# Kernel optimization log

Hardware: AMD Instinct MI355X
Metric: run time of the kernel (lower is better)

The kernel has to match this reference:

```python
import jax, jax.numpy as jnp
import numpy as np

TEMPERATURE = 0.1
NEG_INF = -1e30


def setup_inputs() -> dict:
    key = jax.random.key(0)
    ks = jax.random.split(key, 8)
    T, B, D = 2048, 16, 256
    inp = {
        'q1': jax.random.normal(ks[0], (T, B, D), dtype=jnp.float32),
        'k2': jax.random.normal(ks[1], (T, B, D), dtype=jnp.float32),
        'q2': jax.random.normal(ks[2], (T, B, D), dtype=jnp.float32),
        'k1': jax.random.normal(ks[3], (T, B, D), dtype=jnp.float32),
        'mask_q1': jnp.ones((B, T), dtype=bool),
        'mask_q2': jnp.ones((B, T), dtype=bool),
        'len_q1': jax.random.randint(ks[4], (B,), 0, T, dtype=jnp.int32),
        'len_k2': jax.random.randint(ks[5], (B,), 0, T, dtype=jnp.int32),
        'len_q2': jax.random.randint(ks[6], (B,), 0, T, dtype=jnp.int32),
        'len_k1': jax.random.randint(ks[7], (B,), 0, T, dtype=jnp.int32),
    }
    return inp


def _compute_loss(pred, target, len_pred, len_target):
    # pred, target: (T, B, D) -> (B, T, D)
    pred = jnp.transpose(pred, (1, 0, 2))
    target = jnp.transpose(target, (1, 0, 2))
    B, T, _ = pred.shape
    min_l = jnp.minimum(len_pred, len_target)  # (B,)

    # Batched truncated matmul realized as full matmul + column masking.
    logits = jnp.einsum('btd,bsd->bts', pred, target) / TEMPERATURE  # (B, T, T)
    idx = jnp.arange(T)
    col_valid = idx[None, None, :] < min_l[:, None, None]
    logits = jnp.where(col_valid, logits, NEG_INF)

    # Cross-entropy with labels = arange(min_l): loss_i = lse_i - logits[i, i]
    lse = jax.nn.logsumexp(logits, axis=-1)                 # (B, T)
    diag = jnp.diagonal(logits, axis1=1, axis2=2)           # (B, T)
    row_loss = lse - diag

    row_valid = idx[None, :] < min_l[:, None]               # (B, T)
    denom = jnp.maximum(min_l, 1).astype(pred.dtype)
    per_sample = jnp.sum(jnp.where(row_valid, row_loss, 0.0), axis=1) / denom

    valid = min_l > 0
    n_valid = jnp.sum(valid.astype(pred.dtype))
    total = jnp.sum(jnp.where(valid, per_sample, 0.0))
    return jnp.where(n_valid > 0, total / jnp.maximum(n_valid, 1.0), 0.0)


def reference(q1, k2, q2, k1, mask_q1, mask_q2, len_q1, len_k2, len_q2, len_k1):
    # masks are unused in the original math (kept for interface fidelity)
    loss_a = _compute_loss(q1, k2, len_q1, len_k2)
    loss_b = _compute_loss(q2, k1, len_q2, len_k1)
    return (loss_a + loss_b) / 2
```

## Files before the change

### kernel.cpp

```cpp
#include <hip/hip_runtime.h>
#include <hip/hip_bf16.h>
#include <cmath>

#define T_DIM 2048
#define B_DIM 16
#define D_DIM 256
#define BD (B_DIM * D_DIM)
#define ROWU 256
#define SLAB (T_DIM * ROWU)
#define BM 128
#define BN 64
#define NS 8
#define CHUNK (T_DIM / NS)
#define NEG_INF_F (-1e30f)
#define SCALE_LOG2 14.4269504088896f
#define LN2F 0.6931471805599453f

typedef __attribute__((ext_vector_type(8))) short bf16x8;
typedef __attribute__((ext_vector_type(8))) unsigned short ushort8;
typedef __attribute__((ext_vector_type(4))) float f32x4;

static __device__ __forceinline__ ushort f2bf(float f) {
    union { float f; unsigned int u; } x; x.f = f;
    unsigned int r = (x.u + 0x7FFFu + ((x.u >> 16) & 1u)) >> 16;
    return (ushort)r;
}

static __device__ __forceinline__ void gload_lds16(const ushort* g, ushort* l) {
    __builtin_amdgcn_global_load_lds(
        (const __attribute__((address_space(1))) unsigned int*)g,
        (__attribute__((address_space(3))) unsigned int*)l,
        16, 0, 0);
}

__global__ __launch_bounds__(256) void convert_kernel(
    const float* __restrict__ q1, const float* __restrict__ k2,
    const float* __restrict__ q2, const float* __restrict__ k1,
    const int* __restrict__ lq1, const int* __restrict__ lk2,
    const int* __restrict__ lq2, const int* __restrict__ lk1,
    ushort* __restrict__ wsbf)
{
    const int idx    = blockIdx.x * 256 + threadIdx.x;
    const int tensor = idx >> 20;
    const int rem    = idx & 1048575;
    const int t      = rem >> 9;
    const int r2     = rem & 511;
    const int b      = r2 >> 5;
    const int d8     = (r2 & 31) * 8;
    const int m = (tensor < 2) ? min(lq1[b], lk2[b]) : min(lq2[b], lk1[b]);
    if (t >= m) return;

    const float* src = (tensor == 0) ? q1 : (tensor == 1) ? k2 : (tensor == 2) ? q2 : k1;
    const float scale = (tensor == 0 || tensor == 2) ? SCALE_LOG2 : 1.0f;
    const size_t off = (size_t)t * BD + (size_t)b * D_DIM + d8;
    const float4 v0 = *reinterpret_cast<const float4*>(&src[off]);
    const float4 v1 = *reinterpret_cast<const float4*>(&src[off + 4]);
    ushort8 h;
    h[0] = f2bf(v0.x * scale); h[1] = f2bf(v0.y * scale);
    h[2] = f2bf(v0.z * scale); h[3] = f2bf(v0.w * scale);
    h[4] = f2bf(v1.x * scale); h[5] = f2bf(v1.y * scale);
    h[6] = f2bf(v1.z * scale); h[7] = f2bf(v1.w * scale);
    ushort* dst = &wsbf[(size_t)(tensor * B_DIM + b) * SLAB + (size_t)t * ROWU
                        + (d8 ^ ((t & 15) << 3))];
    *reinterpret_cast<ushort8*>(dst) = h;
}

__global__ __launch_bounds__(256) void partial_lse_bf_kernel(
    const ushort* __restrict__ wsbf,
    const int* __restrict__ len_q1, const int* __restrict__ len_k2,
    const int* __restrict__ len_q2, const int* __restrict__ len_k1,
    float2* __restrict__ partial, float* __restrict__ diag)
{
    const int pair = blockIdx.z / NS;
    const int sc   = blockIdx.z % NS;
    const int b    = blockIdx.y;
    const int t0   = blockIdx.x * BM;

    const int lp = (pair == 0) ? len_q1[b] : len_q2[b];
    const int lt = (pair == 0) ? len_k2[b] : len_k1[b];
    const int m  = min(lp, lt);
    const int s_start = sc * CHUNK;
    if (t0 >= m || s_start >= m) return;
    const int s_hi = min(m, s_start + CHUNK);
    const int pb = pair * B_DIM + b;

    const ushort* pred = wsbf + (size_t)((pair ? 2 : 0) * B_DIM + b) * SLAB;
    const ushort* targ = wsbf + (size_t)((pair ? 3 : 1) * B_DIM + b) * SLAB;

    __shared__ ushort tls[2 * BN * ROWU];

    const int tid = threadIdx.x;
    const int w   = tid >> 6;
    const int l   = tid & 63;
    const int c   = l & 15;
    const int g   = l >> 4;

    #pragma unroll
    for (int q = 0; q < 16; ++q) {
        const int chunk16 = q * 4 + w;
        gload_lds16(&pred[(size_t)t0 * ROWU + chunk16 * 512 + l * 8],
                    &tls[chunk16 * 512]);
    }
    __syncthreads();

    bf16x8 afrag[2][8];
    #pragma unroll
    for (int i = 0; i < 2; ++i) {
        const int ar = 32 * w + 16 * i + c;
        #pragma unroll
        for (int kk = 0; kk < 8; ++kk) {
            const int d = g * 8 + kk * 32;
            afrag[i][kk] = *reinterpret_cast<const bf16x8*>(&tls[(ar << 8) + (d ^ (c << 3))]);
        }
    }
    __syncthreads();

    const int nstage = (s_hi - s_start + BN - 1) / BN;
    #pragma unroll
    for (int q = 0; q < 8; ++q) {
        const int chunk16 = q * 4 + w;
        gload_lds16(&targ[(size_t)s_start * ROWU + chunk16 * 512 + l * 8],
                    &tls[chunk16 * 512]);
    }
    if (nstage > 1) {
        #pragma unroll
        for (int q = 0; q < 8; ++q) {
            const int chunk16 = q * 4 + w;
            gload_lds16(&targ[(size_t)(s_start + BN) * ROWU + chunk16 * 512 + l * 8],
                        &tls[BN * ROWU + chunk16 * 512]);
        }
    }

    float tmax[2][4], tsum[2][4], dg[2][4];
    #pragma unroll
    for (int i = 0; i < 2; ++i)
        #pragma unroll
        for (int rr = 0; rr < 4; ++rr) {
            tmax[i][rr] = NEG_INF_F; tsum[i][rr] = 0.0f; dg[i][rr] = NEG_INF_F;
        }

    __syncthreads();
    int cur = 0;

    for (int st = 0; st < nstage; ++st) {
        const int s0 = s_start + st * BN;
        if (st + 2 < nstage + 1 && st + 1 < nstage && st >= 1) {  }

        if (st >= 1 && st + 1 < nstage) {
            const int nxt = cur ^ 1;
            #pragma unroll
            for (int q = 0; q < 8; ++q) {
                const int chunk16 = q * 4 + w;
                gload_lds16(&targ[(size_t)(s0 + BN) * ROWU + chunk16 * 512 + l * 8],
                            &tls[nxt * (BN * ROWU) + chunk16 * 512]);
            }
        }

        const ushort* buf = &tls[cur * (BN * ROWU)];
        f32x4 acc[2][4];
        #pragma unroll
        for (int i = 0; i < 2; ++i)
            #pragma unroll
            for (int j = 0; j < 4; ++j)
                acc[i][j] = (f32x4){0.f, 0.f, 0.f, 0.f};

        #pragma unroll
        for (int kk = 0; kk < 8; ++kk) {
            bf16x8 bfrag[4];
            #pragma unroll
            for (int j = 0; j < 4; ++j) {
                const int r = 16 * j + c;
                const int d = g * 8 + kk * 32;
                bfrag[j] = *reinterpret_cast<const bf16x8*>(&buf[(r << 8) + (d ^ (c << 3))]);
            }
            #pragma unroll
            for (int i = 0; i < 2; ++i)
                #pragma unroll
                for (int j = 0; j < 4; ++j)
                    acc[i][j] = __builtin_amdgcn_mfma_f32_16x16x32_bf16(
                        afrag[i][kk], bfrag[j], acc[i][j], 0, 0, 0);
        }

        #pragma unroll
        for (int i = 0; i < 2; ++i) {
            #pragma unroll
            for (int rr = 0; rr < 4; ++rr) {
                const int trow = t0 + 32 * w + 16 * i + 4 * g + rr;
                float lg[4];
                float cmax = NEG_INF_F;
                #pragma unroll
                for (int j = 0; j < 4; ++j) {
                    const int s = s0 + 16 * j + c;
                    float v = acc[i][j][rr];
                    v = (s < m) ? v : NEG_INF_F;
                    if (s == trow) dg[i][rr] = v;
                    lg[j] = v;
                    cmax = fmaxf(cmax, v);
                }
                const float nmax = fmaxf(tmax[i][rr], cmax);
                const float add = exp2f(lg[0] - nmax) + exp2f(lg[1] - nmax)
                                + exp2f(lg[2] - nmax) + exp2f(lg[3] - nmax);
                tsum[i][rr] = tsum[i][rr] * exp2f(tmax[i][rr] - nmax) + add;
                tmax[i][rr] = nmax;
            }
        }

        __syncthreads();
        cur ^= 1;
    }

    const bool own_diag = (t0 >= s_start) && (t0 + BM <= s_start + CHUNK);
    #pragma unroll
    for (int i = 0; i < 2; ++i) {
        #pragma unroll
        for (int rr = 0; rr < 4; ++rr) {
            float M = tmax[i][rr], S = tsum[i][rr];
            #pragma unroll
            for (int msk = 1; msk < 16; msk <<= 1) {
                const float Mo = __shfl_xor(M, msk, 64);
                const float So = __shfl_xor(S, msk, 64);
                const float nM = fmaxf(M, Mo);
                S = S * exp2f(M - nM) + So * exp2f(Mo - nM);
                M = nM;
            }
            float d = dg[i][rr];
            #pragma unroll
            for (int msk = 1; msk < 16; msk <<= 1)
                d = fmaxf(d, __shfl_xor(d, msk, 64));
            if (c == 0) {
                const int trow = t0 + 32 * w + 16 * i + 4 * g + rr;
                partial[((size_t)(pb << 11) + trow) * NS + sc] = make_float2(M, S);
                if (own_diag) diag[(pb << 11) + trow] = d;
            }
        }
    }
}

__global__ __launch_bounds__(256) void partial_lse_f32_kernel(
    const float* __restrict__ q1, const float* __restrict__ k2,
    const float* __restrict__ q2, const float* __restrict__ k1,
    const int* __restrict__ len_q1, const int* __restrict__ len_k2,
    const int* __restrict__ len_q2, const int* __restrict__ len_k1,
    float2* __restrict__ partial, float* __restrict__ diag,
    int chunk, int ns)
{
    const int pair = blockIdx.z / ns;
    const int sc   = blockIdx.z % ns;
    const int b    = blockIdx.y;
    const int t0   = blockIdx.x * 128;

    const float* pred = (pair == 0) ? q1 : q2;
    const float* targ = (pair == 0) ? k2 : k1;
    const int lp = (pair == 0) ? len_q1[b] : len_q2[b];
    const int lt = (pair == 0) ? len_k2[b] : len_k1[b];
    const int m  = min(lp, lt);
    const int s_start = sc * chunk;
    if (t0 >= m || s_start >= m) return;
    const int s_hi = min(m, s_start + chunk);
    const int pb = pair * B_DIM + b;

    __shared__ ushort tlf[BN * 256];

    const int tid = threadIdx.x;
    const int w   = tid >> 6;
    const int l   = tid & 63;
    const int c   = l & 15;
    const int g   = l >> 4;

    bf16x8 afrag[2][8];
    #pragma unroll
    for (int i = 0; i < 2; ++i) {
        const float* base = &pred[(size_t)(t0 + 32 * w + 16 * i + c) * BD + (size_t)b * D_DIM];
        #pragma unroll
        for (int kk = 0; kk < 8; ++kk) {
            const int d = g * 8 + kk * 32;
            const float4 v0 = *reinterpret_cast<const float4*>(base + d);
            const float4 v1 = *reinterpret_cast<const float4*>(base + d + 4);
            bf16x8 av;
            av[0] = (short)f2bf(v0.x * SCALE_LOG2); av[1] = (short)f2bf(v0.y * SCALE_LOG2);
            av[2] = (short)f2bf(v0.z * SCALE_LOG2); av[3] = (short)f2bf(v0.w * SCALE_LOG2);
            av[4] = (short)f2bf(v1.x * SCALE_LOG2); av[5] = (short)f2bf(v1.y * SCALE_LOG2);
            av[6] = (short)f2bf(v1.z * SCALE_LOG2); av[7] = (short)f2bf(v1.w * SCALE_LOG2);
            afrag[i][kk] = av;
        }
    }

    float tmax[2][4], tsum[2][4], dg[2][4];
    #pragma unroll
    for (int i = 0; i < 2; ++i)
        #pragma unroll
        for (int rr = 0; rr < 4; ++rr) {
            tmax[i][rr] = NEG_INF_F; tsum[i][rr] = 0.0f; dg[i][rr] = NEG_INF_F;
        }

    for (int s0 = s_start; s0 < s_hi; s0 += BN) {
        __syncthreads();
        #pragma unroll
        for (int v = 0; v < 16; ++v) {
            const int f  = v * 256 + tid;
            const int r  = f >> 6;
            const int d0 = (f & 63) * 4;
            const float4 vv = *reinterpret_cast<const float4*>(
                &targ[(size_t)(s0 + r) * BD + (size_t)b * D_DIM + d0]);
            ushort4 h;
            h.x = f2bf(vv.x); h.y = f2bf(vv.y); h.z = f2bf(vv.z); h.w = f2bf(vv.w);
            *reinterpret_cast<ushort4*>(&tlf[(r << 8) + (d0 ^ ((r & 15) << 3))]) = h;
        }
        __syncthreads();

        f32x4 acc[2][4];
        #pragma unroll
        for (int i = 0; i < 2; ++i)
            #pragma unroll
            for (int j = 0; j < 4; ++j)
                acc[i][j] = (f32x4){0.f, 0.f, 0.f, 0.f};

        #pragma unroll
        for (int kk = 0; kk < 8; ++kk) {
            bf16x8 bfrag[4];
            #pragma unroll
            for (int j = 0; j < 4; ++j) {
                const int r = 16 * j + c;
                const int d = g * 8 + kk * 32;
                bfrag[j] = *reinterpret_cast<const bf16x8*>(&tlf[(r << 8) + (d ^ (c << 3))]);
            }
            #pragma unroll
            for (int i = 0; i < 2; ++i)
                #pragma unroll
                for (int j = 0; j < 4; ++j)
                    acc[i][j] = __builtin_amdgcn_mfma_f32_16x16x32_bf16(
                        afrag[i][kk], bfrag[j], acc[i][j], 0, 0, 0);
        }

        #pragma unroll
        for (int i = 0; i < 2; ++i) {
            #pragma unroll
            for (int rr = 0; rr < 4; ++rr) {
                const int trow = t0 + 32 * w + 16 * i + 4 * g + rr;
                float lg[4];
                float cmax = NEG_INF_F;
                #pragma unroll
                for (int j = 0; j < 4; ++j) {
                    const int s = s0 + 16 * j + c;
                    float v = acc[i][j][rr];
                    v = (s < m) ? v : NEG_INF_F;
                    if (s == trow) dg[i][rr] = v;
                    lg[j] = v;
                    cmax = fmaxf(cmax, v);
                }
                const float nmax = fmaxf(tmax[i][rr], cmax);
                const float add = exp2f(lg[0] - nmax) + exp2f(lg[1] - nmax)
                                + exp2f(lg[2] - nmax) + exp2f(lg[3] - nmax);
                tsum[i][rr] = tsum[i][rr] * exp2f(tmax[i][rr] - nmax) + add;
                tmax[i][rr] = nmax;
            }
        }
    }

    const bool own_diag = (t0 >= s_start) && (t0 + 128 <= s_start + chunk);
    #pragma unroll
    for (int i = 0; i < 2; ++i) {
        #pragma unroll
        for (int rr = 0; rr < 4; ++rr) {
            float M = tmax[i][rr], S = tsum[i][rr];
            #pragma unroll
            for (int msk = 1; msk < 16; msk <<= 1) {
                const float Mo = __shfl_xor(M, msk, 64);
                const float So = __shfl_xor(S, msk, 64);
                const float nM = fmaxf(M, Mo);
                S = S * exp2f(M - nM) + So * exp2f(Mo - nM);
                M = nM;
            }
            float d = dg[i][rr];
            #pragma unroll
            for (int msk = 1; msk < 16; msk <<= 1)
                d = fmaxf(d, __shfl_xor(d, msk, 64));
            if (c == 0) {
                const int trow = t0 + 32 * w + 16 * i + 4 * g + rr;
                partial[((size_t)(pb << 11) + trow) * ns + sc] = make_float2(M, S);
                if (own_diag) diag[(pb << 11) + trow] = d;
            }
        }
    }
}

__global__ __launch_bounds__(256) void combine_kernel(
    const int* __restrict__ len_q1, const int* __restrict__ len_k2,
    const int* __restrict__ len_q2, const int* __restrict__ len_k1,
    const float2* __restrict__ partial, const float* __restrict__ diag,
    float* __restrict__ per_sample, int chunk, int stride)
{
    const int pb   = blockIdx.x;
    const int pair = pb >> 4;
    const int b    = pb & 15;
    const int lp = (pair == 0) ? len_q1[b] : len_q2[b];
    const int lt = (pair == 0) ? len_k2[b] : len_k1[b];
    const int m  = min(lp, lt);

    float local = 0.0f;
    if (m > 0) {
        const int nch = (m + chunk - 1) / chunk;
        for (int t = threadIdx.x; t < m; t += 256) {
            float M = NEG_INF_F, S = 0.0f;
            for (int e = 0; e < nch; ++e) {
                const float2 p = partial[((size_t)(pb << 11) + t) * stride + e];
                const float nM = fmaxf(M, p.x);
                S = S * exp2f(M - nM) + p.y * exp2f(p.x - nM);
                M = nM;
            }
            local += LN2F * ((__log2f(S) + M) - diag[(pb << 11) + t]);
        }
    }

    __shared__ float ws4[4];
    #pragma unroll
    for (int msk = 1; msk < 64; msk <<= 1)
        local += __shfl_xor(local, msk, 64);
    if ((threadIdx.x & 63) == 0) ws4[threadIdx.x >> 6] = local;
    __syncthreads();
    if (threadIdx.x == 0) {
        const float tot = ws4[0] + ws4[1] + ws4[2] + ws4[3];
        per_sample[pb] = (m > 0) ? (tot / (float)m) : 0.0f;
    }
}

__global__ void finalize_kernel(
    const int* __restrict__ len_q1, const int* __restrict__ len_k2,
    const int* __restrict__ len_q2, const int* __restrict__ len_k1,
    const float* __restrict__ per_sample, float* __restrict__ out)
{
    if (threadIdx.x != 0 || blockIdx.x != 0) return;
    float losses[2];
    #pragma unroll
    for (int p = 0; p < 2; ++p) {
        float tot = 0.0f, nv = 0.0f;
        for (int b = 0; b < B_DIM; ++b) {
            const int lp = (p == 0) ? len_q1[b] : len_q2[b];
            const int lt = (p == 0) ? len_k2[b] : len_k1[b];
            const int mm = min(lp, lt);
            if (mm > 0) { tot += per_sample[p * B_DIM + b]; nv += 1.0f; }
        }
        losses[p] = (nv > 0.0f) ? (tot / nv) : 0.0f;
    }
    out[0] = 0.5f * (losses[0] + losses[1]);
}

extern "C" void kernel_launch(void* const* d_in, const int* in_sizes, int n_in,
                              void* d_out, int out_size, void* d_ws, size_t ws_size,
                              hipStream_t stream) {
    const float* q1 = (const float*)d_in[0];
    const float* k2 = (const float*)d_in[1];
    const float* q2 = (const float*)d_in[2];
    const float* k1 = (const float*)d_in[3];
    const int* lq1 = (const int*)d_in[6];
    const int* lk2 = (const int*)d_in[7];
    const int* lq2 = (const int*)d_in[8];
    const int* lk1 = (const int*)d_in[9];
    float* out = (float*)d_out;

    const size_t rows = (size_t)2 * B_DIM * T_DIM;
    const size_t bfbytes = (size_t)4 * B_DIM * SLAB * sizeof(ushort);
    const size_t pbytes  = rows * NS * sizeof(float2);
    const size_t need_pre = bfbytes + pbytes + rows * sizeof(float) + 256;

    if (ws_size >= need_pre) {
        ushort* wsbf       = (ushort*)d_ws;
        float2* partial    = (float2*)((char*)d_ws + bfbytes);
        float*  diag       = (float*)((char*)partial + pbytes);
        float*  per_sample = diag + rows;

        convert_kernel<<<16384, 256, 0, stream>>>(q1, k2, q2, k1, lq1, lk2, lq2, lk1, wsbf);

        dim3 gridA(T_DIM / BM, B_DIM, 2 * NS);
        partial_lse_bf_kernel<<<gridA, 256, 0, stream>>>(
            wsbf, lq1, lk2, lq2, lk1, partial, diag);

        combine_kernel<<<32, 256, 0, stream>>>(
            lq1, lk2, lq2, lk1, partial, diag, per_sample, CHUNK, NS);
        finalize_kernel<<<1, 64, 0, stream>>>(lq1, lk2, lq2, lk1, per_sample, out);
    } else {
        int ns = 8;
        while (ns > 1) {
            const size_t need = rows * ns * sizeof(float2) + rows * sizeof(float) + 256;
            if (need <= ws_size) break;
            ns >>= 1;
        }
        const int chunk = T_DIM / ns;
        float2* partial    = (float2*)d_ws;
        float*  diag       = (float*)((char*)d_ws + rows * ns * sizeof(float2));
        float*  per_sample = diag + rows;

        dim3 gridA(T_DIM / 128, B_DIM, 2 * ns);
        partial_lse_f32_kernel<<<gridA, 256, 0, stream>>>(
            q1, k2, q2, k1, lq1, lk2, lq2, lk1, partial, diag, chunk, ns);

        combine_kernel<<<32, 256, 0, stream>>>(
            lq1, lk2, lq2, lk1, partial, diag, per_sample, chunk, ns);
        finalize_kernel<<<1, 64, 0, stream>>>(lq1, lk2, lq2, lk1, per_sample, out);
    }
}
```

Baseline: 90.12 us.

## Deepen target tile pipeline to four buffers and remap blocks across XCDs

The main bf16 partial-LSE kernel now streams 32-row target tiles through a four-deep LDS ring with explicit vmcnt waits and one barrier per stage, replacing the double-buffered 64-row scheme with two barriers per stage. The A fragments are loaded straight from global memory instead of being staged through LDS, and the grid is flattened to 1D with a block-index swizzle that spreads work across XCDs. The aim is better overlap of loads with MFMA work and better cache locality. The cost is smaller MFMA tiles per stage, more loop iterations, and reliance on hand-counted vmcnt values.

```diff
diff --git a/kernel.cpp b/kernel.cpp
--- a/kernel.cpp
+++ b/kernel.cpp
@@ -9,7 +9,8 @@
 #define ROWU 256
 #define SLAB (T_DIM * ROWU)
 #define BM 128
-#define BN 64
+#define BN 32
+#define NBUF 4
 #define NS 8
 #define CHUNK (T_DIM / NS)
 #define NEG_INF_F (-1e30f)
@@ -71,10 +72,14 @@
     const int* __restrict__ len_q2, const int* __restrict__ len_k1,
     float2* __restrict__ partial, float* __restrict__ diag)
 {
-    const int pair = blockIdx.z / NS;
-    const int sc   = blockIdx.z % NS;
-    const int b    = blockIdx.y;
-    const int t0   = blockIdx.x * BM;
+    const int h   = blockIdx.x;
+    const int lin = (h & 7) * 512 + (h >> 3);
+    const int bx   = lin & 15;
+    const int b    = (lin >> 4) & 15;
+    const int z    = lin >> 8;
+    const int pair = z >> 3;
+    const int sc   = z & 7;
+    const int t0   = bx * BM;
 
     const int lp = (pair == 0) ? len_q1[b] : len_q2[b];
     const int lt = (pair == 0) ? len_k2[b] : len_k1[b];
@@ -87,7 +92,7 @@
     const ushort* pred = wsbf + (size_t)((pair ? 2 : 0) * B_DIM + b) * SLAB;
     const ushort* targ = wsbf + (size_t)((pair ? 3 : 1) * B_DIM + b) * SLAB;
 
-    __shared__ ushort tls[2 * BN * ROWU];
+    __shared__ ushort tls[NBUF * BN * ROWU];
 
     const int tid = threadIdx.x;
     const int w   = tid >> 6;
@@ -95,41 +100,32 @@
     const int c   = l & 15;
     const int g   = l >> 4;
 
-    #pragma unroll
-    for (int q = 0; q < 16; ++q) {
-        const int chunk16 = q * 4 + w;
-        gload_lds16(&pred[(size_t)t0 * ROWU + chunk16 * 512 + l * 8],
-                    &tls[chunk16 * 512]);
-    }
-    __syncthreads();
-
     bf16x8 afrag[2][8];
     #pragma unroll
     for (int i = 0; i < 2; ++i) {
-        const int ar = 32 * w + 16 * i + c;
+        const ushort* base = &pred[(size_t)(t0 + 32 * w + 16 * i + c) * ROWU];
         #pragma unroll
         for (int kk = 0; kk < 8; ++kk) {
             const int d = g * 8 + kk * 32;
-            afrag[i][kk] = *reinterpret_cast<const bf16x8*>(&tls[(ar << 8) + (d ^ (c << 3))]);
-        }
-    }
-    __syncthreads();
+            afrag[i][kk] = *reinterpret_cast<const bf16x8*>(&base[d ^ (c << 3)]);
+        }
+    }
 
     const int nstage = (s_hi - s_start + BN - 1) / BN;
-    #pragma unroll
-    for (int q = 0; q < 8; ++q) {
-        const int chunk16 = q * 4 + w;
-        gload_lds16(&targ[(size_t)s_start * ROWU + chunk16 * 512 + l * 8],
-                    &tls[chunk16 * 512]);
-    }
-    if (nstage > 1) {
-        #pragma unroll
-        for (int q = 0; q < 8; ++q) {
-            const int chunk16 = q * 4 + w;
-            gload_lds16(&targ[(size_t)(s_start + BN) * ROWU + chunk16 * 512 + l * 8],
-                        &tls[BN * ROWU + chunk16 * 512]);
-        }
-    }
+
+#define ISSUE_STAGE(st_) do {                                                  \
+        const ushort* _src = targ + (size_t)(s_start + (st_) * BN) * ROWU;     \
+        ushort* _dst = &tls[((st_) & (NBUF - 1)) * (BN * ROWU)];               \
+        _Pragma("unroll")                                                      \
+        for (int q = 0; q < 4; ++q)                                            \
+            gload_lds16(_src + (q * 4 + w) * 512 + l * 8,                      \
+                        _dst + (q * 4 + w) * 512);                             \
+    } while (0)
+
+    int issued = (nstage < 3) ? nstage : 3;
+    if (issued > 0) ISSUE_STAGE(0);
+    if (issued > 1) ISSUE_STAGE(1);
+    if (issued > 2) ISSUE_STAGE(2);
 
     float tmax[2][4], tsum[2][4], dg[2][4];
     #pragma unroll
@@ -139,24 +135,159 @@
             tmax[i][rr] = NEG_INF_F; tsum[i][rr] = 0.0f; dg[i][rr] = NEG_INF_F;
         }
 
-    __syncthreads();
-    int cur = 0;
-
     for (int st = 0; st < nstage; ++st) {
+        const int remn = issued - st - 1;
+        if (remn >= 2)      asm volatile("s_waitcnt vmcnt(8)" ::: "memory");
+        else if (remn == 1) asm volatile("s_waitcnt vmcnt(4)" ::: "memory");
+        else                asm volatile("s_waitcnt vmcnt(0)" ::: "memory");
+        __builtin_amdgcn_sched_barrier(0);
+        __builtin_amdgcn_s_barrier();
+        __builtin_amdgcn_sched_barrier(0);
+
+        if (st + 3 < nstage) { ISSUE_STAGE(st + 3); ++issued; }
+
+        const ushort* buf = &tls[(st & (NBUF - 1)) * (BN * ROWU)];
         const int s0 = s_start + st * BN;
-        if (st + 2 < nstage + 1 && st + 1 < nstage && st >= 1) {  }
-
-        if (st >= 1 && st + 1 < nstage) {
-            const int nxt = cur ^ 1;
-            #pragma unroll
-            for (int q = 0; q < 8; ++q) {
-                const int chunk16 = q * 4 + w;
-                gload_lds16(&targ[(size_t)(s0 + BN) * ROWU + chunk16 * 512 + l * 8],
-                            &tls[nxt * (BN * ROWU) + chunk16 * 512]);
-            }
-        }
-
-        const ushort* buf = &tls[cur * (BN * ROWU)];
+
+        f32x4 acc[2][2];
+        #pragma unroll
+        for (int i = 0; i < 2; ++i)
+            #pragma unroll
+            for (int j = 0; j < 2; ++j)
+                acc[i][j] = (f32x4){0.f, 0.f, 0.f, 0.f};
+
+        #pragma unroll
+        for (int kk = 0; kk < 8; ++kk) {
+            const int d = g * 8 + kk * 32;
+            const bf16x8 b0 = *reinterpret_cast<const bf16x8*>(
+                &buf[(c << 8) + (d ^ (c << 3))]);
+            const bf16x8 b1 = *reinterpret_cast<const bf16x8*>(
+                &buf[((16 + c) << 8) + (d ^ (c << 3))]);
+            acc[0][0] = __builtin_amdgcn_mfma_f32_16x16x32_bf16(afrag[0][kk], b0, acc[0][0], 0, 0, 0);
+            acc[0][1] = __builtin_amdgcn_mfma_f32_16x16x32_bf16(afrag[0][kk], b1, acc[0][1], 0, 0, 0);
+            acc[1][0] = __builtin_amdgcn_mfma_f32_16x16x32_bf16(afrag[1][kk], b0, acc[1][0], 0, 0, 0);
+            acc[1][1] = __builtin_amdgcn_mfma_f32_16x16x32_bf16(afrag[1][kk], b1, acc[1][1], 0, 0, 0);
+        }
+
+        #pragma unroll
+        for (int i = 0; i < 2; ++i) {
+            #pragma unroll
+            for (int rr = 0; rr < 4; ++rr) {
+                const int trow = t0 + 32 * w + 16 * i + 4 * g + rr;
+                const int s0c  = s0 + c;
+                float v0 = (s0c      < m) ? acc[i][0][rr] : NEG_INF_F;
+                float v1 = (s0c + 16 < m) ? acc[i][1][rr] : NEG_INF_F;
+                if (s0c      == trow) dg[i][rr] = v0;
+                if (s0c + 16 == trow) dg[i][rr] = v1;
+                const float cmax = fmaxf(v0, v1);
+                const float nmax = fmaxf(tmax[i][rr], cmax);
+                const float add  = exp2f(v0 - nmax) + exp2f(v1 - nmax);
+                tsum[i][rr] = tsum[i][rr] * exp2f(tmax[i][rr] - nmax) + add;
+                tmax[i][rr] = nmax;
+            }
+        }
+    }
+#undef ISSUE_STAGE
+
+    const bool own_diag = (t0 >= s_start) && (t0 + BM <= s_start + CHUNK);
+    #pragma unroll
+    for (int i = 0; i < 2; ++i) {
+        #pragma unroll
+        for (int rr = 0; rr < 4; ++rr) {
+            float M = tmax[i][rr], S = tsum[i][rr];
+            #pragma unroll
+            for (int msk = 1; msk < 16; msk <<= 1) {
+                const float Mo = __shfl_xor(M, msk, 64);
+                const float So = __shfl_xor(S, msk, 64);
+                const float nM = fmaxf(M, Mo);
+                S = S * exp2f(M - nM) + So * exp2f(Mo - nM);
+                M = nM;
+            }
+            float d = dg[i][rr];
+            #pragma unroll
+            for (int msk = 1; msk < 16; msk <<= 1)
+                d = fmaxf(d, __shfl_xor(d, msk, 64));
+            if (c == 0) {
+                const int trow = t0 + 32 * w + 16 * i + 4 * g + rr;
+                partial[((size_t)(pb << 11) + trow) * NS + sc] = make_float2(M, S);
+                if (own_diag) diag[(pb << 11) + trow] = d;
+            }
+        }
+    }
+}
+
+__global__ __launch_bounds__(256) void partial_lse_f32_kernel(
+    const float* __restrict__ q1, const float* __restrict__ k2,
+    const float* __restrict__ q2, const float* __restrict__ k1,
+    const int* __restrict__ len_q1, const int* __restrict__ len_k2,
+    const int* __restrict__ len_q2, const int* __restrict__ len_k1,
+    float2* __restrict__ partial, float* __restrict__ diag,
+    int chunk, int ns)
+{
+    const int pair = blockIdx.z / ns;
+    const int sc   = blockIdx.z % ns;
+    const int b    = blockIdx.y;
+    const int t0   = blockIdx.x * 128;
+
+    const float* pred = (pair == 0) ? q1 : q2;
+    const float* targ = (pair == 0) ? k2 : k1;
+    const int lp = (pair == 0) ? len_q1[b] : len_q2[b];
+    const int lt = (pair == 0) ? len_k2[b] : len_k1[b];
+    const int m  = min(lp, lt);
+    const int s_start = sc * chunk;
+    if (t0 >= m || s_start >= m) return;
+    const int s_hi = min(m, s_start + chunk);
+    const int pb = pair * B_DIM + b;
+
+    __shared__ ushort tlf[64 * 256];
+
+    const int tid = threadIdx.x;
+    const int w   = tid >> 6;
+    const int l   = tid & 63;
+    const int c   = l & 15;
+    const int g   = l >> 4;
+
+    bf16x8 afrag[2][8];
+    #pragma unroll
+    for (int i = 0; i < 2; ++i) {
+        const float* base = &pred[(size_t)(t0 + 32 * w + 16 * i + c) * BD + (size_t)b * D_DIM];
+        #pragma unroll
+        for (int kk = 0; kk < 8; ++kk) {
+            const int d = g * 8 + kk * 32;
+            const float4 v0 = *reinterpret_cast<const float4*>(base + d);
+            const float4 v1 = *reinterpret_cast<const float4*>(base + d + 4);
+            bf16x8 av;
+            av[0] = (short)f2bf(v0.x * SCALE_LOG2); av[1] = (short)f2bf(v0.y * SCALE_LOG2);
+            av[2] = (short)f2bf(v0.z * SCALE_LOG2); av[3] = (short)f2bf(v0.w * SCALE_LOG2);
+            av[4] = (short)f2bf(v1.x * SCALE_LOG2); av[5] = (short)f2bf(v1.y * SCALE_LOG2);
+            av[6] = (short)f2bf(v1.z * SCALE_LOG2); av[7] = (short)f2bf(v1.w * SCALE_LOG2);
+            afrag[i][kk] = av;
+        }
+    }
+
+    float tmax[2][4], tsum[2][4], dg[2][4];
+    #pragma unroll
+    for (int i = 0; i < 2; ++i)
+        #pragma unroll
+        for (int rr = 0; rr < 4; ++rr) {
+            tmax[i][rr] = NEG_INF_F; tsum[i][rr] = 0.0f; dg[i][rr] = NEG_INF_F;
+        }
+
+    for (int s0 = s_start; s0 < s_hi; s0 += 64) {
+        __syncthreads();
+        #pragma unroll
+        for (int v = 0; v < 16; ++v) {
+            const int f  = v * 256 + tid;
+            const int r  = f >> 6;
+            const int d0 = (f & 63) * 4;
+            const float4 vv = *reinterpret_cast<const float4*>(
+                &targ[(size_t)(s0 + r) * BD + (size_t)b * D_DIM + d0]);
+            ushort4 hh;
+            hh.x = f2bf(vv.x); hh.y = f2bf(vv.y); hh.z = f2bf(vv.z); hh.w = f2bf(vv.w);
+            *reinterpret_cast<ushort4*>(&tlf[(r << 8) + (d0 ^ ((r & 15) << 3))]) = hh;
+        }
+        __syncthreads();
+
         f32x4 acc[2][4];
         #pragma unroll
         for (int i = 0; i < 2; ++i)
@@ -171,7 +302,7 @@
             for (int j = 0; j < 4; ++j) {
                 const int r = 16 * j + c;
                 const int d = g * 8 + kk * 32;
-                bfrag[j] = *reinterpret_cast<const bf16x8*>(&buf[(r << 8) + (d ^ (c << 3))]);
+                bfrag[j] = *reinterpret_cast<const bf16x8*>(&tlf[(r << 8) + (d ^ (c << 3))]);
             }
             #pragma unroll
             for (int i = 0; i < 2; ++i)
@@ -204,157 +335,6 @@
                 tmax[i][rr] = nmax;
             }
         }
-
-        __syncthreads();
-        cur ^= 1;
-    }
-
-    const bool own_diag = (t0 >= s_start) && (t0 + BM <= s_start + CHUNK);
-    #pragma unroll
-    for (int i = 0; i < 2; ++i) {
-        #pragma unroll
-        for (int rr = 0; rr < 4; ++rr) {
-            float M = tmax[i][rr], S = tsum[i][rr];
-            #pragma unroll
-            for (int msk = 1; msk < 16; msk <<= 1) {
-                const float Mo = __shfl_xor(M, msk, 64);
-                const float So = __shfl_xor(S, msk, 64);
-                const float nM = fmaxf(M, Mo);
-                S = S * exp2f(M - nM) + So * exp2f(Mo - nM);
-                M = nM;
-            }
-            float d = dg[i][rr];
-            #pragma unroll
-            for (int msk = 1; msk < 16; msk <<= 1)
-                d = fmaxf(d, __shfl_xor(d, msk, 64));
-            if (c == 0) {
-                const int trow = t0 + 32 * w + 16 * i + 4 * g + rr;
-                partial[((size_t)(pb << 11) + trow) * NS + sc] = make_float2(M, S);
-                if (own_diag) diag[(pb << 11) + trow] = d;
-            }
-        }
-    }
-}
-
-__global__ __launch_bounds__(256) void partial_lse_f32_kernel(
-    const float* __restrict__ q1, const float* __restrict__ k2,
-    const float* __restrict__ q2, const float* __restrict__ k1,
-    const int* __restrict__ len_q1, const int* __restrict__ len_k2,
-    const int* __restrict__ len_q2, const int* __restrict__ len_k1,
-    float2* __restrict__ partial, float* __restrict__ diag,
-    int chunk, int ns)
-{
-    const int pair = blockIdx.z / ns;
-    const int sc   = blockIdx.z % ns;
-    const int b    = blockIdx.y;
-    const int t0   = blockIdx.x * 128;
-
-    const float* pred = (pair == 0) ? q1 : q2;
-    const float* targ = (pair == 0) ? k2 : k1;
-    const int lp = (pair == 0) ? len_q1[b] : len_q2[b];
-    const int lt = (pair == 0) ? len_k2[b] : len_k1[b];
-    const int m  = min(lp, lt);
-    const int s_start = sc * chunk;
-    if (t0 >= m || s_start >= m) return;
-    const int s_hi = min(m, s_start + chunk);
-    const int pb = pair * B_DIM + b;
-
-    __shared__ ushort tlf[BN * 256];
-
-    const int tid = threadIdx.x;
-    const int w   = tid >> 6;
-    const int l   = tid & 63;
-    const int c   = l & 15;
-    const int g   = l >> 4;
-
-    bf16x8 afrag[2][8];
-    #pragma unroll
-    for (int i = 0; i < 2; ++i) {
-        const float* base = &pred[(size_t)(t0 + 32 * w + 16 * i + c) * BD + (size_t)b * D_DIM];
-        #pragma unroll
-        for (int kk = 0; kk < 8; ++kk) {
-            const int d = g * 8 + kk * 32;
-            const float4 v0 = *reinterpret_cast<const float4*>(base + d);
-            const float4 v1 = *reinterpret_cast<const float4*>(base + d + 4);
-            bf16x8 av;
-            av[0] = (short)f2bf(v0.x * SCALE_LOG2); av[1] = (short)f2bf(v0.y * SCALE_LOG2);
-            av[2] = (short)f2bf(v0.z * SCALE_LOG2); av[3] = (short)f2bf(v0.w * SCALE_LOG2);
-            av[4] = (short)f2bf(v1.x * SCALE_LOG2); av[5] = (short)f2bf(v1.y * SCALE_LOG2);
-            av[6] = (short)f2bf(v1.z * SCALE_LOG2); av[7] = (short)f2bf(v1.w * SCALE_LOG2);
-            afrag[i][kk] = av;
-        }
-    }
-
-    float tmax[2][4], tsum[2][4], dg[2][4];
-    #pragma unroll
-    for (int i = 0; i < 2; ++i)
-        #pragma unroll
-        for (int rr = 0; rr < 4; ++rr) {
-            tmax[i][rr] = NEG_INF_F; tsum[i][rr] = 0.0f; dg[i][rr] = NEG_INF_F;
-        }
-
-    for (int s0 = s_start; s0 < s_hi; s0 += BN) {
-        __syncthreads();
-        #pragma unroll
-        for (int v = 0; v < 16; ++v) {
-            const int f  = v * 256 + tid;
-            const int r  = f >> 6;
-            const int d0 = (f & 63) * 4;
-            const float4 vv = *reinterpret_cast<const float4*>(
-                &targ[(size_t)(s0 + r) * BD + (size_t)b * D_DIM + d0]);
-            ushort4 h;
-            h.x = f2bf(vv.x); h.y = f2bf(vv.y); h.z = f2bf(vv.z); h.w = f2bf(vv.w);
-            *reinterpret_cast<ushort4*>(&tlf[(r << 8) + (d0 ^ ((r & 15) << 3))]) = h;
-        }
-        __syncthreads();
-
-        f32x4 acc[2][4];
-        #pragma unroll
-        for (int i = 0; i < 2; ++i)
-            #pragma unroll
-            for (int j = 0; j < 4; ++j)
-                acc[i][j] = (f32x4){0.f, 0.f, 0.f, 0.f};
-
-        #pragma unroll
-        for (int kk = 0; kk < 8; ++kk) {
-            bf16x8 bfrag[4];
-            #pragma unroll
-            for (int j = 0; j < 4; ++j) {
-                const int r = 16 * j + c;
-                const int d = g * 8 + kk * 32;
-                bfrag[j] = *reinterpret_cast<const bf16x8*>(&tlf[(r << 8) + (d ^ (c << 3))]);
-            }
-            #pragma unroll
-            for (int i = 0; i < 2; ++i)
-                #pragma unroll
-                for (int j = 0; j < 4; ++j)
-                    acc[i][j] = __builtin_amdgcn_mfma_f32_16x16x32_bf16(
-                        afrag[i][kk], bfrag[j], acc[i][j], 0, 0, 0);
-        }
-
-        #pragma unroll
-        for (int i = 0; i < 2; ++i) {
-            #pragma unroll
-            for (int rr = 0; rr < 4; ++rr) {
-                const int trow = t0 + 32 * w + 16 * i + 4 * g + rr;
-                float lg[4];
-                float cmax = NEG_INF_F;
-                #pragma unroll
-                for (int j = 0; j < 4; ++j) {
-                    const int s = s0 + 16 * j + c;
-                    float v = acc[i][j][rr];
-                    v = (s < m) ? v : NEG_INF_F;
-                    if (s == trow) dg[i][rr] = v;
-                    lg[j] = v;
-                    cmax = fmaxf(cmax, v);
-                }
-                const float nmax = fmaxf(tmax[i][rr], cmax);
-                const float add = exp2f(lg[0] - nmax) + exp2f(lg[1] - nmax)
-                                + exp2f(lg[2] - nmax) + exp2f(lg[3] - nmax);
-                tsum[i][rr] = tsum[i][rr] * exp2f(tmax[i][rr] - nmax) + add;
-                tmax[i][rr] = nmax;
-            }
-        }
     }
 
     const bool own_diag = (t0 >= s_start) && (t0 + 128 <= s_start + chunk);
@@ -471,8 +451,7 @@
 
         convert_kernel<<<16384, 256, 0, stream>>>(q1, k2, q2, k1, lq1, lk2, lq2, lk1, wsbf);
 
-        dim3 gridA(T_DIM / BM, B_DIM, 2 * NS);
-        partial_lse_bf_kernel<<<gridA, 256, 0, stream>>>(
+        partial_lse_bf_kernel<<<4096, 256, 0, stream>>>(
             wsbf, lq1, lk2, lq2, lk1, partial, diag);
 
         combine_kernel<<<32, 256, 0, stream>>>(
```

New measurement: 98.81 us. 1.1x slower.
